# Kernel optimization log

Measured on AMD Instinct MI355X. Metric: run time of the kernel, lower is better.

## Reference

```python
import jax, jax.numpy as jnp
import numpy as np

N = 100000   # nodes (single node type)
E = 160000   # edges per relation
R = 4        # relations
D_IN = 128
D_OUT = 128


def setup_inputs() -> dict:
    key = jax.random.key(0)
    k_x, k_w, k_lw, k_s, k_d = jax.random.split(key, 5)
    x = jax.random.normal(k_x, (N, D_IN), dtype=jnp.float32)
    # xavier-ish scale for weights
    scale = np.float32(np.sqrt(2.0 / (D_IN + D_OUT)))
    W = jax.random.normal(k_w, (R, D_IN, D_OUT), dtype=jnp.float32) * scale
    loop_weight = jax.random.normal(k_lw, (D_IN, D_OUT), dtype=jnp.float32) * scale
    src = jax.random.randint(k_s, (R, E), 0, N, dtype=jnp.int64)
    dst = jax.random.randint(k_d, (R, E), 0, N, dtype=jnp.int64)
    return {"x": x, "W": W, "loop_weight": loop_weight, "src": src, "dst": dst}


def reference(x, W, loop_weight, src, dst):
    # Per-relation linear transform: [R, N, D_OUT]
    h = jnp.einsum('nd,rde->rne', x, W)

    def rel_aggregate(hr, s, d):
        # gather messages at src, sum into dst, normalize by dst in-degree ('right' norm)
        msg = hr[s]                                            # [E, D_OUT]
        agg = jax.ops.segment_sum(msg, d, num_segments=N)      # [N, D_OUT]
        deg = jax.ops.segment_sum(jnp.ones(s.shape, hr.dtype), d, num_segments=N)
        return agg / jnp.clip(deg, 1.0)[:, None]

    per_rel = jax.vmap(rel_aggregate)(h, src, dst)             # [R, N, D_OUT]
    out = per_rel.sum(axis=0) + x @ loop_weight                # sum over relations + self-loop
    return jax.nn.relu(out)                                    # activation; dropout=0 -> identity
```

## Files before the change

### kernel.cpp

```cpp
#include <hip/hip_runtime.h>

#define D 128
#define TN 64
#define NC 8

typedef __attribute__((ext_vector_type(8))) short short8;
typedef __attribute__((ext_vector_type(4))) float f32x4;

__device__ __forceinline__ unsigned int bf16rne(float f) {
  unsigned int b = __float_as_uint(f);
  return (b + 0x7fffu + ((b >> 16) & 1u)) >> 16;
}
__device__ __forceinline__ float bf2f(unsigned int u) {
  return __uint_as_float(u << 16);
}

__global__ __launch_bounds__(256) void rgc_prep_w(
    const float* __restrict__ W, const float* __restrict__ loopW,
    unsigned short* __restrict__ WT, int R)
{
  int tid = blockIdx.x * 256 + threadIdx.x;
  int s = tid >> 14;
  if (s > R) return;
  int rem = tid & 16383;
  int k = rem >> 7;
  int c = rem & 127;
  float v = (s < R) ? W[(size_t)s * D * D + k * D + c] : loopW[k * D + c];
  unsigned int u = bf16rne(v);
  unsigned int off = ((unsigned int)(c * D + k) * 2u) ^ (((unsigned int)(c & 7)) << 4);
  *(unsigned short*)((char*)WT + (size_t)s * D * D * 2 + off) = (unsigned short)u;
}

__global__ __launch_bounds__(256) void rgc_prep_x(
    const float* __restrict__ x, unsigned short* __restrict__ xb, long long total8)
{
  long long i = (long long)blockIdx.x * 256 + threadIdx.x;
  if (i >= total8) return;
  float4 v0 = ((const float4*)x)[i * 2];
  float4 v1 = ((const float4*)x)[i * 2 + 1];
  uint4 u;
  u.x = bf16rne(v0.x) | (bf16rne(v0.y) << 16);
  u.y = bf16rne(v0.z) | (bf16rne(v0.w) << 16);
  u.z = bf16rne(v1.x) | (bf16rne(v1.y) << 16);
  u.w = bf16rne(v1.z) | (bf16rne(v1.w) << 16);
  ((uint4*)xb)[i] = u;
}

__global__ __launch_bounds__(256) void rgc_hist(
    const int* __restrict__ dst, int* __restrict__ cnt8, int N, int E, int R)
{
  int r = blockIdx.y;
  int e = blockIdx.x * 256 + threadIdx.x;
  if (e >= E) return;
  int k = (blockIdx.x + gridDim.x * blockIdx.y) & (NC - 1);
  int d = dst[(size_t)r * E + e];
  atomicAdd(&cnt8[((size_t)k * R + r) * N + d], 1);
}

__global__ __launch_bounds__(256) void rgc_offsets(
    const int* __restrict__ cnt8, int* __restrict__ rowctr8,
    int* __restrict__ off8, int* __restrict__ nodeptr, int* __restrict__ degv,
    int N, int E, int R, int ntiles, int nchunks)
{
  int wv = threadIdx.x >> 6, lane = threadIdx.x & 63;
  int chunk = blockIdx.x * 4 + wv;
  if (chunk >= nchunks) return;
  int kx = blockIdx.x & (NC - 1);
  int r = chunk / ntiles, tile = chunk - r * ntiles;
  int node = tile * TN + lane;

  int ck[NC];
  int deg = 0;
  if (node < N) {
#pragma unroll
    for (int k = 0; k < NC; k++) {
      ck[k] = cnt8[((size_t)k * R + r) * N + node];
      deg += ck[k];
    }
  } else {
#pragma unroll
    for (int k = 0; k < NC; k++) ck[k] = 0;
  }
  int v = deg;
#pragma unroll
  for (int o = 1; o < 64; o <<= 1) {
    int t = __shfl_up(v, o, 64);
    if (lane >= o) v += t;
  }
  int total = __shfl(v, 63, 64);
  int base = 0;
  if (lane == 0) base = atomicAdd(&rowctr8[kx * R + r], total);
  base = __shfl(base, 0, 64);
  int start = (kx * R + r) * E + base + (v - deg);

  if (node < N) {
    nodeptr[(size_t)r * N + node] = start;
    degv[(size_t)r * N + node] = deg;
    int run = start;
#pragma unroll
    for (int k = 0; k < NC; k++) {
      off8[((size_t)k * R + r) * N + node] = run;
      run += ck[k];
    }
  }
}

__global__ __launch_bounds__(256) void rgc_fill(
    const int* __restrict__ src, const int* __restrict__ dst,
    int* __restrict__ off8, int* __restrict__ esrc, int N, int E, int R)
{
  int r = blockIdx.y;
  int e = blockIdx.x * 256 + threadIdx.x;
  if (e >= E) return;
  int k = (blockIdx.x + gridDim.x * blockIdx.y) & (NC - 1);
  int d = dst[(size_t)r * E + e];
  int pos = atomicAdd(&off8[((size_t)k * R + r) * N + d], 1);
  esrc[pos] = src[(size_t)r * E + e];
}

__global__ __launch_bounds__(256) void rgc_agg(
    const unsigned short* __restrict__ xb, const int* __restrict__ nodeptr,
    const int* __restrict__ degv, const int* __restrict__ esrc,
    unsigned short* __restrict__ Ahat, int N, int R, int ntiles)
{
  int tx = threadIdx.x;
  int tile = blockIdx.x;
  int r = blockIdx.y;
  int node0 = tile * TN;
  int grp = tx >> 4, c = tx & 15;
  char* dstp = (char*)(Ahat + ((size_t)tile * R + r) * (TN * D));

#pragma unroll
  for (int t = 0; t < 4; t++) {
    int row = grp * 4 + t;
    int node = node0 + row;
    float a[8];
#pragma unroll
    for (int q = 0; q < 8; q++) a[q] = 0.f;
    int deg = 0;
    if (node < N) {
      int st = nodeptr[(size_t)r * N + node];
      deg = degv[(size_t)r * N + node];
      for (int j = 0; j < deg; j++) {
        int s = esrc[st + j];
        uint4 u = ((const uint4*)(xb + (size_t)s * D))[c];
        a[0] += bf2f(u.x & 0xffffu); a[1] += bf2f(u.x >> 16);
        a[2] += bf2f(u.y & 0xffffu); a[3] += bf2f(u.y >> 16);
        a[4] += bf2f(u.z & 0xffffu); a[5] += bf2f(u.z >> 16);
        a[6] += bf2f(u.w & 0xffffu); a[7] += bf2f(u.w >> 16);
      }
    }
    float sc = 1.0f / fmaxf((float)deg, 1.0f);
    uint4 o;
    o.x = bf16rne(a[0] * sc) | (bf16rne(a[1] * sc) << 16);
    o.y = bf16rne(a[2] * sc) | (bf16rne(a[3] * sc) << 16);
    o.z = bf16rne(a[4] * sc) | (bf16rne(a[5] * sc) << 16);
    o.w = bf16rne(a[6] * sc) | (bf16rne(a[7] * sc) << 16);
    unsigned int off =
        ((unsigned int)(row * 256 + c * 16)) ^ (((unsigned int)(row & 7)) << 4);
    *(uint4*)(dstp + off) = o;
  }
}

__global__ __launch_bounds__(256) void rgc_gemm(
    const unsigned short* __restrict__ xb, const unsigned short* __restrict__ WT,
    const unsigned short* __restrict__ Ahat, float* __restrict__ out,
    int N, int R, int ntiles)
{
  __shared__ char Ab[TN * D * 2];
  __shared__ char Wb[D * D * 2];

  int tx = threadIdx.x;
  int tile = blockIdx.x;
  int node0 = tile * TN;
  int lane = tx & 63;
  int w = tx >> 6;

  f32x4 acc[8];
#pragma unroll
  for (int i = 0; i < 8; i++) acc[i] = (f32x4){0.f, 0.f, 0.f, 0.f};

  for (int s = 0; s <= R; s++) {
    bool is_loop = (s == R);
    if (!is_loop) {
      const float4* asrc = (const float4*)(Ahat + ((size_t)tile * R + s) * (TN * D));
#pragma unroll
      for (int i = 0; i < 4; i++)
        ((float4*)Ab)[tx + i * 256] = asrc[tx + i * 256];
    } else {
#pragma unroll
      for (int it = 0; it < 4; it++) {
        int i = tx + it * 256;
        int row = i >> 4, c16 = i & 15;
        int node = node0 + row;
        uint4 u = make_uint4(0, 0, 0, 0);
        if (node < N) u = ((const uint4*)(xb + (size_t)node * D))[c16];
        unsigned int off =
            ((unsigned int)(row * 256 + c16 * 16)) ^ (((unsigned int)(row & 7)) << 4);
        *(uint4*)(Ab + off) = u;
      }
    }
    const float4* wsrc = (const float4*)(WT + (size_t)s * D * D);
#pragma unroll
    for (int i = 0; i < 8; i++)
      ((float4*)Wb)[tx + i * 256] = wsrc[tx + i * 256];
    __syncthreads();

    int rA = w * 16 + (lane & 15);
    unsigned int mA = (unsigned int)((rA & 7) << 4);
    unsigned int kof = (unsigned int)((lane >> 4) * 16);
    short8 afr[4];
#pragma unroll
    for (int kk = 0; kk < 4; kk++)
      afr[kk] = *(const short8*)(Ab + rA * 256 + (((unsigned int)(kk * 64) + kof) ^ mA));
#pragma unroll
    for (int ct = 0; ct < 8; ct++) {
      int rB = ct * 16 + (lane & 15);
      unsigned int mB = (unsigned int)((rB & 7) << 4);
#pragma unroll
      for (int kk = 0; kk < 4; kk++) {
        short8 b = *(const short8*)(Wb + rB * 256 + (((unsigned int)(kk * 64) + kof) ^ mB));
        acc[ct] = __builtin_amdgcn_mfma_f32_16x16x32_bf16(afr[kk], b, acc[ct], 0, 0, 0);
      }
    }
    __syncthreads();
  }

  int colb = lane & 15;
  int rowb = (lane >> 4) * 4;
#pragma unroll
  for (int ct = 0; ct < 8; ct++) {
#pragma unroll
    for (int j = 0; j < 4; j++) {
      int node = node0 + w * 16 + rowb + j;
      if (node < N)
        out[(size_t)node * D + ct * 16 + colb] = fmaxf(acc[ct][j], 0.f);
    }
  }
}

extern "C" void kernel_launch(void* const* d_in, const int* in_sizes, int n_in,
                              void* d_out, int out_size, void* d_ws, size_t ws_size,
                              hipStream_t stream)
{
  const float* x     = (const float*)d_in[0];
  const float* W     = (const float*)d_in[1];
  const float* loopW = (const float*)d_in[2];
  const int*   src   = (const int*)d_in[3];
  const int*   dst   = (const int*)d_in[4];
  float* out = (float*)d_out;

  int N = in_sizes[0] / D;
  int R = in_sizes[1] / (D * D);
  int E = in_sizes[3] / R;
  int ntiles = (N + TN - 1) / TN;

  size_t o_cnt8  = 0;
  size_t o_rowc  = o_cnt8 + (size_t)NC * R * N * 4;
  size_t o_off8  = (o_rowc + (size_t)NC * R * 4 + 15) & ~(size_t)15;
  size_t o_np    = (o_off8 + (size_t)NC * R * N * 4 + 15) & ~(size_t)15;
  size_t o_deg   = (o_np + (size_t)R * N * 4 + 15) & ~(size_t)15;
  size_t o_esrc  = (o_deg + (size_t)R * N * 4 + 15) & ~(size_t)15;
  size_t o_wt    = (o_esrc + (size_t)NC * R * E * 4 + 15) & ~(size_t)15;
  size_t o_xb    = (o_wt + (size_t)(R + 1) * D * D * 2 + 15) & ~(size_t)15;
  size_t o_ahat  = (o_xb + (size_t)N * D * 2 + 15) & ~(size_t)15;

  char* wsb = (char*)d_ws;
  int*  cnt8    = (int*)(wsb + o_cnt8);
  int*  rowctr8 = (int*)(wsb + o_rowc);
  int*  off8    = (int*)(wsb + o_off8);
  int*  nodeptr = (int*)(wsb + o_np);
  int*  degv    = (int*)(wsb + o_deg);
  int*  esrc    = (int*)(wsb + o_esrc);
  unsigned short* WT   = (unsigned short*)(wsb + o_wt);
  unsigned short* xb   = (unsigned short*)(wsb + o_xb);
  unsigned short* Ahat = (unsigned short*)(wsb + o_ahat);

  rgc_prep_w<<<((R + 1) * D * D + 255) / 256, 256, 0, stream>>>(W, loopW, WT, R);
  long long total8 = (long long)N * D / 8;
  rgc_prep_x<<<(int)((total8 + 255) / 256), 256, 0, stream>>>(x, xb, total8);

  hipMemsetAsync(cnt8, 0, (size_t)NC * R * N * 4 + (size_t)NC * R * 4, stream);
  dim3 egrid((E + 255) / 256, R);
  rgc_hist<<<egrid, 256, 0, stream>>>(dst, cnt8, N, E, R);
  int nchunks = R * ntiles;
  rgc_offsets<<<(nchunks + 3) / 4, 256, 0, stream>>>(
      cnt8, rowctr8, off8, nodeptr, degv, N, E, R, ntiles, nchunks);
  rgc_fill<<<egrid, 256, 0, stream>>>(src, dst, off8, esrc, N, E, R);

  dim3 agrid(ntiles, R);
  rgc_agg<<<agrid, 256, 0, stream>>>(xb, nodeptr, degv, esrc, Ahat, N, R, ntiles);
  rgc_gemm<<<ntiles, 256, 0, stream>>>(xb, WT, Ahat, out, N, R, ntiles);
}
```

Baseline: 212.4 us.

## Chunk agg+gemm for L2 reuse, drop LDS staging in gemm, merge prep kernels

Splits the aggregation and GEMM stages into two node chunks so each chunk's Ahat intermediate is smaller and more likely to stay in cache between the two kernels, with Ahat indexed per local tile. The GEMM now loads A and W fragments directly from global memory into registers instead of staging them through shared memory, which removes both __syncthreads. The two prep kernels are merged into one launch. The trade-off is more launches for agg/gemm, plus uncoalesced, repeated global reads of W across blocks, which now depend on cache.

New measurement: 270.5 us. 1.27x slower.

```diff
diff --git a/kernel.cpp b/kernel.cpp
--- a/kernel.cpp
+++ b/kernel.cpp
@@ -3,6 +3,7 @@
 #define D 128
 #define TN 64
 #define NC 8
+#define NCHK 2
 
 typedef __attribute__((ext_vector_type(8))) short short8;
 typedef __attribute__((ext_vector_type(4))) float f32x4;
@@ -15,35 +16,34 @@
   return __uint_as_float(u << 16);
 }
 
-__global__ __launch_bounds__(256) void rgc_prep_w(
-    const float* __restrict__ W, const float* __restrict__ loopW,
-    unsigned short* __restrict__ WT, int R)
-{
-  int tid = blockIdx.x * 256 + threadIdx.x;
-  int s = tid >> 14;
-  if (s > R) return;
-  int rem = tid & 16383;
-  int k = rem >> 7;
-  int c = rem & 127;
-  float v = (s < R) ? W[(size_t)s * D * D + k * D + c] : loopW[k * D + c];
-  unsigned int u = bf16rne(v);
-  unsigned int off = ((unsigned int)(c * D + k) * 2u) ^ (((unsigned int)(c & 7)) << 4);
-  *(unsigned short*)((char*)WT + (size_t)s * D * D * 2 + off) = (unsigned short)u;
-}
-
-__global__ __launch_bounds__(256) void rgc_prep_x(
-    const float* __restrict__ x, unsigned short* __restrict__ xb, long long total8)
-{
-  long long i = (long long)blockIdx.x * 256 + threadIdx.x;
-  if (i >= total8) return;
-  float4 v0 = ((const float4*)x)[i * 2];
-  float4 v1 = ((const float4*)x)[i * 2 + 1];
-  uint4 u;
-  u.x = bf16rne(v0.x) | (bf16rne(v0.y) << 16);
-  u.y = bf16rne(v0.z) | (bf16rne(v0.w) << 16);
-  u.z = bf16rne(v1.x) | (bf16rne(v1.y) << 16);
-  u.w = bf16rne(v1.z) | (bf16rne(v1.w) << 16);
-  ((uint4*)xb)[i] = u;
+__global__ __launch_bounds__(256) void rgc_prep(
+    const float* __restrict__ x, const float* __restrict__ W,
+    const float* __restrict__ loopW, unsigned short* __restrict__ xb,
+    unsigned short* __restrict__ WT, int R, long long total8, int xblocks)
+{
+  if ((int)blockIdx.x < xblocks) {
+    long long i = (long long)blockIdx.x * 256 + threadIdx.x;
+    if (i >= total8) return;
+    float4 v0 = ((const float4*)x)[i * 2];
+    float4 v1 = ((const float4*)x)[i * 2 + 1];
+    uint4 u;
+    u.x = bf16rne(v0.x) | (bf16rne(v0.y) << 16);
+    u.y = bf16rne(v0.z) | (bf16rne(v0.w) << 16);
+    u.z = bf16rne(v1.x) | (bf16rne(v1.y) << 16);
+    u.w = bf16rne(v1.z) | (bf16rne(v1.w) << 16);
+    ((uint4*)xb)[i] = u;
+  } else {
+    int tid = (blockIdx.x - xblocks) * 256 + threadIdx.x;
+    int s = tid >> 14;
+    if (s > R) return;
+    int rem = tid & 16383;
+    int k = rem >> 7;
+    int c = rem & 127;
+    float v = (s < R) ? W[(size_t)s * D * D + k * D + c] : loopW[k * D + c];
+    unsigned int u = bf16rne(v);
+    unsigned int off = ((unsigned int)(c * D + k) * 2u) ^ (((unsigned int)(c & 7)) << 4);
+    *(unsigned short*)((char*)WT + (size_t)s * D * D * 2 + off) = (unsigned short)u;
+  }
 }
 
 __global__ __launch_bounds__(256) void rgc_hist(
@@ -121,14 +121,15 @@
 __global__ __launch_bounds__(256) void rgc_agg(
     const unsigned short* __restrict__ xb, const int* __restrict__ nodeptr,
     const int* __restrict__ degv, const int* __restrict__ esrc,
-    unsigned short* __restrict__ Ahat, int N, int R, int ntiles)
+    unsigned short* __restrict__ Ahat, int N, int R, int tile0)
 {
   int tx = threadIdx.x;
-  int tile = blockIdx.x;
+  int ltile = blockIdx.x;
+  int tile = tile0 + ltile;
   int r = blockIdx.y;
   int node0 = tile * TN;
   int grp = tx >> 4, c = tx & 15;
-  char* dstp = (char*)(Ahat + ((size_t)tile * R + r) * (TN * D));
+  char* dstp = (char*)(Ahat + ((size_t)ltile * R + r) * (TN * D));
 
 #pragma unroll
   for (int t = 0; t < 4; t++) {
@@ -165,13 +166,11 @@
 __global__ __launch_bounds__(256) void rgc_gemm(
     const unsigned short* __restrict__ xb, const unsigned short* __restrict__ WT,
     const unsigned short* __restrict__ Ahat, float* __restrict__ out,
-    int N, int R, int ntiles)
-{
-  __shared__ char Ab[TN * D * 2];
-  __shared__ char Wb[D * D * 2];
-
+    int N, int R, int tile0)
+{
   int tx = threadIdx.x;
-  int tile = blockIdx.x;
+  int ltile = blockIdx.x;
+  int tile = tile0 + ltile;
   int node0 = tile * TN;
   int lane = tx & 63;
   int w = tx >> 6;
@@ -180,50 +179,39 @@
 #pragma unroll
   for (int i = 0; i < 8; i++) acc[i] = (f32x4){0.f, 0.f, 0.f, 0.f};
 
+  int rA = w * 16 + (lane & 15);
+  unsigned int mA = (unsigned int)((rA & 7) << 4);
+  unsigned int kof = (unsigned int)((lane >> 4) * 16);
+
   for (int s = 0; s <= R; s++) {
-    bool is_loop = (s == R);
-    if (!is_loop) {
-      const float4* asrc = (const float4*)(Ahat + ((size_t)tile * R + s) * (TN * D));
-#pragma unroll
-      for (int i = 0; i < 4; i++)
-        ((float4*)Ab)[tx + i * 256] = asrc[tx + i * 256];
+    short8 afr[4];
+    if (s < R) {
+      const char* abase = (const char*)(Ahat + ((size_t)ltile * R + s) * (TN * D));
+#pragma unroll
+      for (int kk = 0; kk < 4; kk++)
+        afr[kk] = *(const short8*)(abase + rA * 256 +
+                                   (((unsigned int)(kk * 64) + kof) ^ mA));
     } else {
-#pragma unroll
-      for (int it = 0; it < 4; it++) {
-        int i = tx + it * 256;
-        int row = i >> 4, c16 = i & 15;
-        int node = node0 + row;
-        uint4 u = make_uint4(0, 0, 0, 0);
-        if (node < N) u = ((const uint4*)(xb + (size_t)node * D))[c16];
-        unsigned int off =
-            ((unsigned int)(row * 256 + c16 * 16)) ^ (((unsigned int)(row & 7)) << 4);
-        *(uint4*)(Ab + off) = u;
+      const char* xrow = (const char*)(xb + (size_t)(node0 + rA) * D);
+      bool ok = (node0 + rA) < N;
+#pragma unroll
+      for (int kk = 0; kk < 4; kk++) {
+        short8 z = {0, 0, 0, 0, 0, 0, 0, 0};
+        afr[kk] = ok ? *(const short8*)(xrow + kk * 64 + kof) : z;
       }
     }
-    const float4* wsrc = (const float4*)(WT + (size_t)s * D * D);
-#pragma unroll
-    for (int i = 0; i < 8; i++)
-      ((float4*)Wb)[tx + i * 256] = wsrc[tx + i * 256];
-    __syncthreads();
-
-    int rA = w * 16 + (lane & 15);
-    unsigned int mA = (unsigned int)((rA & 7) << 4);
-    unsigned int kof = (unsigned int)((lane >> 4) * 16);
-    short8 afr[4];
-#pragma unroll
-    for (int kk = 0; kk < 4; kk++)
-      afr[kk] = *(const short8*)(Ab + rA * 256 + (((unsigned int)(kk * 64) + kof) ^ mA));
+    const char* wbase = (const char*)(WT + (size_t)s * D * D);
 #pragma unroll
     for (int ct = 0; ct < 8; ct++) {
       int rB = ct * 16 + (lane & 15);
       unsigned int mB = (unsigned int)((rB & 7) << 4);
 #pragma unroll
       for (int kk = 0; kk < 4; kk++) {
-        short8 b = *(const short8*)(Wb + rB * 256 + (((unsigned int)(kk * 64) + kof) ^ mB));
+        short8 b = *(const short8*)(wbase + rB * 256 +
+                                    (((unsigned int)(kk * 64) + kof) ^ mB));
         acc[ct] = __builtin_amdgcn_mfma_f32_16x16x32_bf16(afr[kk], b, acc[ct], 0, 0, 0);
       }
     }
-    __syncthreads();
   }
 
   int colb = lane & 15;
@@ -254,6 +242,7 @@
   int R = in_sizes[1] / (D * D);
   int E = in_sizes[3] / R;
   int ntiles = (N + TN - 1) / TN;
+  int ctmax = (ntiles + NCHK - 1) / NCHK;
 
   size_t o_cnt8  = 0;
   size_t o_rowc  = o_cnt8 + (size_t)NC * R * N * 4;
@@ -276,9 +265,10 @@
   unsigned short* xb   = (unsigned short*)(wsb + o_xb);
   unsigned short* Ahat = (unsigned short*)(wsb + o_ahat);
 
-  rgc_prep_w<<<((R + 1) * D * D + 255) / 256, 256, 0, stream>>>(W, loopW, WT, R);
   long long total8 = (long long)N * D / 8;
-  rgc_prep_x<<<(int)((total8 + 255) / 256), 256, 0, stream>>>(x, xb, total8);
+  int xblocks = (int)((total8 + 255) / 256);
+  int wblocks = ((R + 1) * D * D + 255) / 256;
+  rgc_prep<<<xblocks + wblocks, 256, 0, stream>>>(x, W, loopW, xb, WT, R, total8, xblocks);
 
   hipMemsetAsync(cnt8, 0, (size_t)NC * R * N * 4 + (size_t)NC * R * 4, stream);
   dim3 egrid((E + 255) / 256, R);
@@ -288,7 +278,12 @@
       cnt8, rowctr8, off8, nodeptr, degv, N, E, R, ntiles, nchunks);
   rgc_fill<<<egrid, 256, 0, stream>>>(src, dst, off8, esrc, N, E, R);
 
-  dim3 agrid(ntiles, R);
-  rgc_agg<<<agrid, 256, 0, stream>>>(xb, nodeptr, degv, esrc, Ahat, N, R, ntiles);
-  rgc_gemm<<<ntiles, 256, 0, stream>>>(xb, WT, Ahat, out, N, R, ntiles);
-}
+  for (int c = 0; c < NCHK; c++) {
+    int tile0 = c * ctmax;
+    int ct = (ntiles - tile0 < ctmax) ? (ntiles - tile0) : ctmax;
+    if (ct <= 0) break;
+    dim3 agrid(ct, R);
+    rgc_agg<<<agrid, 256, 0, stream>>>(xb, nodeptr, degv, esrc, Ahat, N, R, tile0);
+    rgc_gemm<<<ct, 256, 0, stream>>>(xb, WT, Ahat, out, N, R, tile0);
+  }
+}
```
